# Performance work log

Hardware: AMD Instinct MI355X
Metric: run time of the kernel (lower is better)

Reference implementation:

```python
import math
import jax, jax.numpy as jnp
import numpy as np


def _bilinear_maps_sample(kv_feats, shapes_wh, start_ids, locs, map_ids):
    """Bilinear sampling from concatenated multi-level 2D maps.

    kv_feats: [BH, S, C] flattened (row-major, per level) feature maps
    shapes_wh: [L, 2] int (W, H) per level
    start_ids: [L] int start offset of each level in S
    locs: [BH, M, 2] normalized (x, y) in [0, 1]
    map_ids: [BH, M] int level index per sample
    returns [BH, M, C]
    """
    wh = shapes_wh[map_ids]                      # [BH, M, 2]
    W = wh[..., 0]
    H = wh[..., 1]
    start = start_ids[map_ids]                   # [BH, M]
    Wf = W.astype(locs.dtype)
    Hf = H.astype(locs.dtype)
    x = locs[..., 0] * Wf - 0.5                  # align_corners=False convention
    y = locs[..., 1] * Hf - 0.5
    x0 = jnp.floor(x)
    y0 = jnp.floor(y)
    out = jnp.zeros(locs.shape[:-1] + (kv_feats.shape[-1],), kv_feats.dtype)
    for dx in (0, 1):
        for dy in (0, 1):
            xi = x0 + dx
            yi = y0 + dy
            w = (1.0 - jnp.abs(x - xi)) * (1.0 - jnp.abs(y - yi))
            valid = (xi >= 0) & (xi < Wf) & (yi >= 0) & (yi < Hf)
            xi_c = jnp.clip(xi, 0, Wf - 1).astype(jnp.int32)
            yi_c = jnp.clip(yi, 0, Hf - 1).astype(jnp.int32)
            idx = start + yi_c * W + xi_c        # [BH, M]
            f = jnp.take_along_axis(kv_feats, idx[..., None], axis=1)
            out = out + jnp.where(valid, w, 0.0)[..., None] * f
    return out


def setup_inputs() -> dict:
    key = jax.random.key(0)
    ks = jax.random.split(key, 10)
    B, N, L, Hh, P = 2, 2048, 5, 8, 4
    in_size, sample_size = 256, 256
    qk_size, value_size = 256, 256
    kv_size = qk_size + value_size

    shapes = np.array([[128, 128], [64, 64], [32, 32], [16, 16], [8, 8]], np.int32)  # (H, W)
    flat = (shapes[:, 0] * shapes[:, 1]).astype(np.int64)
    start = np.concatenate([[0], np.cumsum(flat)[:-1]]).astype(np.int32)
    S = int(flat.sum())  # 21824

    # sampling_offsets bias: canonical Deformable-DETR grid init
    thetas = np.arange(Hh, dtype=np.float32) * (2.0 * math.pi / Hh)
    grid = np.stack([np.cos(thetas), np.sin(thetas)], axis=1)
    grid = grid / np.abs(grid).max(axis=1, keepdims=True)
    grid = np.tile(grid.reshape(Hh, 1, 1, 2), (1, L, 1, 1))
    sizes = np.arange(1, P + 1, dtype=np.float32).reshape(1, 1, P, 1)
    b_off = (sizes * grid).reshape(-1)           # [H*L*P*2]

    def lin(k, out_d, in_d):
        return jax.random.normal(k, (out_d, in_d), jnp.float32) * (1.0 / math.sqrt(in_d))

    return {
        "in_feats": jax.random.normal(ks[0], (B, N, in_size), jnp.float32),
        "sample_priors": jax.random.uniform(ks[1], (B, N, L, 2), jnp.float32),
        "sample_feats": jax.random.normal(ks[2], (B, S, sample_size), jnp.float32),
        "sample_map_shapes": jnp.asarray(shapes),
        "sample_map_start_ids": jnp.asarray(start),
        "W_off": jax.random.normal(ks[3], (Hh * L * P * 2, in_size), jnp.float32) * 0.02,
        "b_off": jnp.asarray(b_off),
        "W_q": lin(ks[4], qk_size, in_size),
        "b_q": jnp.zeros((qk_size,), jnp.float32),
        "W_kv": lin(ks[5], kv_size, sample_size),
        "b_kv": jnp.zeros((kv_size,), jnp.float32),
        "point_encs": jax.random.normal(ks[6], (Hh, L * P, qk_size // Hh), jnp.float32) * 0.02,
        "W_out": lin(ks[7], in_size, value_size),
        "b_out": jnp.zeros((in_size,), jnp.float32),
    }


def reference(in_feats, sample_priors, sample_feats, sample_map_shapes,
              sample_map_start_ids, W_off, b_off, W_q, b_q, W_kv, b_kv,
              point_encs, W_out, b_out):
    B, N = in_feats.shape[:2]
    Hh, LP, dqk = point_encs.shape
    L = sample_map_shapes.shape[0]
    P = LP // L

    # sampling offsets + locations (priors last dim == 2 path)
    off = (in_feats @ W_off.T + b_off).reshape(B, N, Hh, L, P, 2)
    shapes_wh = sample_map_shapes[:, ::-1]                      # fliplr -> (W, H)
    norm = shapes_wh.astype(in_feats.dtype)[None, None, None, :, None, :]
    locs = sample_priors[:, :, None, :, None, :] + off / norm    # [B,N,H,L,P,2]

    q = (in_feats @ W_q.T + b_q).reshape(B, N, Hh, dqk)
    kv = sample_feats @ W_kv.T + b_kv                            # [B,S,kv_size]
    ck = kv.shape[-1] // Hh
    kv = kv.reshape(B, -1, Hh, ck).transpose(0, 2, 1, 3).reshape(B * Hh, -1, ck)

    locs = locs.transpose(0, 2, 1, 3, 4, 5).reshape(B * Hh, N * L * P, 2)
    map_ids = jnp.broadcast_to(jnp.arange(L, dtype=jnp.int32)[None, None, :, None],
                               (B * Hh, N, L, P)).reshape(B * Hh, -1)

    sampled = _bilinear_maps_sample(kv, shapes_wh, sample_map_start_ids, locs, map_ids)
    sampled = sampled.reshape(B, Hh, N, LP, ck).transpose(0, 2, 1, 3, 4)  # [B,N,H,LP,ck]

    keys = sampled[..., :dqk] + point_encs                       # [B,N,H,LP,dqk]
    vals = sampled[..., dqk:]                                    # [B,N,H,LP,cv]
    attn = jax.nn.softmax(
        jnp.einsum('bnhd,bnhpd->bnhp', q / math.sqrt(dqk), keys), axis=-1)
    weighted = jnp.einsum('bnhp,bnhpd->bnhd', attn, vals).reshape(B, N, -1)
    return weighted @ W_out.T + b_out
```

## Files before the change

### kernel.cpp

```cpp
#include <hip/hip_runtime.h>
#include <cstddef>

#define B_  2
#define N_  2048
#define L_  5
#define HH  8
#define P_  4
#define S_  21824
#define DQK 32

using bf16x8 = __attribute__((ext_vector_type(8))) short;
using f32x4  = __attribute__((ext_vector_type(4))) float;
using us8    = __attribute__((ext_vector_type(8))) unsigned short;
using h2     = __attribute__((ext_vector_type(2))) _Float16;

__device__ __forceinline__ unsigned short f2b(float f) {
  unsigned u = __builtin_bit_cast(unsigned, f);
  u += 0x7FFFu + ((u >> 16) & 1u);
  return (unsigned short)(u >> 16);
}
__device__ __forceinline__ float b2f(unsigned short h) {
  return __builtin_bit_cast(float, ((unsigned)h) << 16);
}
__device__ __forceinline__ unsigned cvtpk(float lo, float hi) {
  unsigned r;
  asm("v_cvt_pk_bf16_f32 %0, %1, %2" : "=v"(r) : "v"(lo), "v"(hi));
  return r;
}
__device__ __forceinline__ h2 pkrtz(float a, float b) {
  return __builtin_bit_cast(h2, __builtin_amdgcn_cvt_pkrtz(a, b));
}
__device__ __forceinline__ unsigned pkrtz_u(float a, float b) {
  return __builtin_bit_cast(unsigned, __builtin_amdgcn_cvt_pkrtz(a, b));
}
__device__ __forceinline__ h2 u2h(unsigned u) { return __builtin_bit_cast(h2, u); }

__device__ __forceinline__ void gld_lds16(const void* g, void* l) {
  __builtin_amdgcn_global_load_lds(
      (const __attribute__((address_space(1))) unsigned int*)g,
      (__attribute__((address_space(3))) unsigned int*)l, 16, 0, 0);
}

template <int CTRL>
__device__ __forceinline__ float dppadd(float v) {
  const int x = __builtin_bit_cast(int, v);
  return v + __builtin_bit_cast(float,
      __builtin_amdgcn_update_dpp(x, x, CTRL, 0xF, 0xF, false));
}

#define E0 1396736
#define E1 1527808
#define E2 1658880
#define E3 1675264
#define E4 1683456
#define E5 1691648
#define E6 1703936
#define E7 1716224

__device__ __forceinline__ void cvt8_plain(const float* s, unsigned short* d, int u) {
  const float4 a = ((const float4*)s)[2 * u];
  const float4 b = ((const float4*)s)[2 * u + 1];
  us8 o;
  o[0] = f2b(a.x); o[1] = f2b(a.y); o[2] = f2b(a.z); o[3] = f2b(a.w);
  o[4] = f2b(b.x); o[5] = f2b(b.y); o[6] = f2b(b.z); o[7] = f2b(b.w);
  ((us8*)d)[u] = o;
}
__device__ __forceinline__ unsigned short f2b_lo(float x) {
  return f2b(x - b2f(f2b(x)));
}
__device__ __forceinline__ void cvt8_lo(const float* s, unsigned short* d, int u) {
  const float4 a = ((const float4*)s)[2 * u];
  const float4 b = ((const float4*)s)[2 * u + 1];
  us8 o;
  o[0] = f2b_lo(a.x); o[1] = f2b_lo(a.y); o[2] = f2b_lo(a.z); o[3] = f2b_lo(a.w);
  o[4] = f2b_lo(b.x); o[5] = f2b_lo(b.y); o[6] = f2b_lo(b.z); o[7] = f2b_lo(b.w);
  ((us8*)d)[u] = o;
}

__global__ __launch_bounds__(256) void cvt_all(
    const float* __restrict__ sfeats, const float* __restrict__ in_feats,
    const float* __restrict__ W_kv, const float* __restrict__ W_q,
    const float* __restrict__ W_out, const float* __restrict__ W_off,
    unsigned short* __restrict__ sf_bf, unsigned short* __restrict__ if_hi,
    unsigned short* __restrict__ if_lo, unsigned short* __restrict__ wkv_bf,
    unsigned short* __restrict__ wq_bf, unsigned short* __restrict__ wout_bf,
    unsigned short* __restrict__ woff_hi, unsigned short* __restrict__ woff_lo) {
  const int i = blockIdx.x * 256 + threadIdx.x;
  if      (i < E0) cvt8_plain(sfeats, sf_bf, i);
  else if (i < E1) cvt8_plain(in_feats, if_hi, i - E0);
  else if (i < E2) cvt8_lo(in_feats, if_lo, i - E1);
  else if (i < E3) cvt8_plain(W_kv, wkv_bf, i - E2);
  else if (i < E4) cvt8_plain(W_q, wq_bf, i - E3);
  else if (i < E5) cvt8_plain(W_out, wout_bf, i - E4);
  else if (i < E6) {
    const int u = i - E5;
    if ((u >> 5) < 320) cvt8_plain(W_off, woff_hi, u);
    else ((us8*)woff_hi)[u] = (us8)0;
  } else {
    const int u = i - E6;
    if ((u >> 5) < 320) cvt8_lo(W_off, woff_lo, u);
    else ((us8*)woff_lo)[u] = (us8)0;
  }
}

__device__ __forceinline__ void mfma_compute(
    const unsigned short* As, const unsigned short* Bs,
    int wr, int wc, int fr, int fq, f32x4 (&acc)[4][4]) {
#pragma unroll
  for (int kk = 0; kk < 2; ++kk) {
    bf16x8 af[4], bfv[4];
#pragma unroll
    for (int i = 0; i < 4; ++i) {
      const int ar = wr * 64 + i * 16 + fr;
      const int cha = (kk * 4 + fq) ^ (ar & 7);
      af[i] = *(const bf16x8*)(As + ar * 64 + cha * 8);
      const int br = wc * 64 + i * 16 + fr;
      const int chb = (kk * 4 + fq) ^ (br & 7);
      bfv[i] = *(const bf16x8*)(Bs + br * 64 + chb * 8);
    }
#pragma unroll
    for (int i = 0; i < 4; ++i)
#pragma unroll
      for (int j = 0; j < 4; ++j)
        acc[i][j] = __builtin_amdgcn_mfma_f32_16x16x32_bf16(
            af[i], bfv[j], acc[i][j], 0, 0, 0);
  }
}

__device__ __forceinline__ void mfma_tile_bf16(
    const unsigned short* __restrict__ Ap, const unsigned short* __restrict__ Wp,
    unsigned short* As, unsigned short* Bs,
    int row0, int col0, int wv, int wr, int wc, int fr, int fq,
    int srow, int sch, f32x4 (&acc)[4][4]) {
  for (int k0 = 0; k0 < 256; k0 += 64) {
#pragma unroll
    for (int i = 0; i < 4; ++i) {
      const int r = i * 32 + srow;
      const int ca = sch ^ (r & 7);
      gld_lds16(Ap + (size_t)(row0 + r) * 256 + k0 + ca * 8,
                As + (size_t)(i * 32 + wv * 8) * 64);
      gld_lds16(Wp + (size_t)(col0 + r) * 256 + k0 + ca * 8,
                Bs + (size_t)(i * 32 + wv * 8) * 64);
    }
    __syncthreads();
    mfma_compute(As, Bs, wr, wc, fr, fq, acc);
    __syncthreads();
  }
}

__global__ __launch_bounds__(256) void ubergemm(
    const unsigned short* __restrict__ sf_bf,
    const unsigned short* __restrict__ wkv_bf,
    const unsigned short* __restrict__ if_hi,
    const unsigned short* __restrict__ if_lo,
    const unsigned short* __restrict__ woff_hi,
    const unsigned short* __restrict__ woff_lo,
    const unsigned short* __restrict__ wq_bf,
    const float* __restrict__ b_kv, const float* __restrict__ b_off,
    const float* __restrict__ b_q,
    unsigned short* __restrict__ kvt, float* __restrict__ offb,
    float* __restrict__ qb) {
  __shared__ __align__(16) unsigned short lds[128 * 128];

  const int tid = threadIdx.x;
  const int lane = tid & 63;
  const int wv = tid >> 6;
  const int wr = wv >> 1, wc = wv & 1;
  const int fr = lane & 15, fq = lane >> 4;
  const int bx = blockIdx.x;

  f32x4 acc[4][4] = {};

  if (bx >= 160) {
    const int t = bx - 160;
    const int x = t & 7;
    const int idx = t >> 3;
    const int c = idx & 3;
    const int g = (idx >> 2) * 8 + x;
    if (g >= 341) return;
    const int row0 = g * 128;
    const int col0 = c * 128;

    unsigned short* Ab[2] = {lds, lds + 4096};
    unsigned short* Bb[2] = {lds + 8192, lds + 12288};

#define KV_STAGE(KK, BUF)                                                     \
    {                                                                         \
      _Pragma("unroll")                                                       \
      for (int ld = 0; ld < 2; ++ld) {                                        \
        const int ci = ld * 256 + tid;                                        \
        const int rw = ci >> 2, cc = ci & 3;                                  \
        const int ca = cc ^ (rw & 3);                                         \
        gld_lds16(sf_bf + (size_t)(row0 + rw) * 256 + (KK) * 32 + ca * 8,     \
                  Ab[BUF] + (size_t)(ld * 256 + wv * 64) * 8);                \
        gld_lds16(wkv_bf + (size_t)(col0 + rw) * 256 + (KK) * 32 + ca * 8,    \
                  Bb[BUF] + (size_t)(ld * 256 + wv * 64) * 8);                \
      }                                                                       \
    }

    KV_STAGE(0, 0);
#pragma unroll
    for (int k = 0; k < 8; ++k) {
      if (k < 7) {
        KV_STAGE(k + 1, (k + 1) & 1);
        asm volatile("s_waitcnt vmcnt(4)" ::: "memory");
      } else {
        asm volatile("s_waitcnt vmcnt(0)" ::: "memory");
      }
      __builtin_amdgcn_s_barrier();
      __builtin_amdgcn_sched_barrier(0);
      const unsigned short* Ac = Ab[k & 1];
      const unsigned short* Bc = Bb[k & 1];
      bf16x8 af[4], bfv[4];
#pragma unroll
      for (int i = 0; i < 4; ++i) {
        const int ar = wr * 64 + i * 16 + fr;
        af[i] = *(const bf16x8*)(Ac + (ar * 4 + (fq ^ (ar & 3))) * 8);
      }
#pragma unroll
      for (int j = 0; j < 4; ++j) {
        const int nr = wc * 64 + j * 16 + fr;
        bfv[j] = *(const bf16x8*)(Bc + (nr * 4 + (fq ^ (nr & 3))) * 8);
      }
#pragma unroll
      for (int j = 0; j < 4; ++j)
#pragma unroll
        for (int i = 0; i < 4; ++i)
          acc[j][i] = __builtin_amdgcn_mfma_f32_16x16x32_bf16(
              bfv[j], af[i], acc[j][i], 0, 0, 0);
      __builtin_amdgcn_s_barrier();
    }
#undef KV_STAGE

#pragma unroll
    for (int j = 0; j < 4; ++j) {
      const int c0 = col0 + wc * 64 + j * 16 + fq * 4;
      const float4 bb = *(const float4*)(b_kv + c0);
      const int h = c0 >> 6;
      const int cc = c0 & 63;
#pragma unroll
      for (int i = 0; i < 4; ++i) {
        const int sl = row0 + wr * 64 + i * 16 + fr;
        const int b = (sl >= S_) ? 1 : 0;
        const int s = sl - b * S_;
        unsigned* dst = (unsigned*)(kvt + ((size_t)(b * HH + h) * S_ + s) * 64 + cc);
        dst[0] = pkrtz_u(acc[j][i][0] + bb.x, acc[j][i][1] + bb.y);
        dst[1] = pkrtz_u(acc[j][i][2] + bb.z, acc[j][i][3] + bb.w);
      }
    }
    return;
  }

  unsigned short* As = lds;
  unsigned short* Bs = lds + 128 * 64;
  const int srow = tid >> 3;
  const int sch = tid & 7;
  int row0, col0, ldc, nbias;
  const float* bias;
  float* Cf;
  if (bx < 96) {
    col0 = (bx % 3) * 128; row0 = (bx / 3) * 128;
    bias = b_off; Cf = offb; ldc = 384; nbias = 320;
    mfma_tile_bf16(if_hi, woff_hi, As, Bs, row0, col0, wv, wr, wc, fr, fq, srow, sch, acc);
    mfma_tile_bf16(if_hi, woff_lo, As, Bs, row0, col0, wv, wr, wc, fr, fq, srow, sch, acc);
    mfma_tile_bf16(if_lo, woff_hi, As, Bs, row0, col0, wv, wr, wc, fr, fq, srow, sch, acc);
  } else {
    const int t = bx - 96;
    col0 = (t & 1) * 128; row0 = (t >> 1) * 128;
    bias = b_q; Cf = qb; ldc = 256; nbias = 256;
    mfma_tile_bf16(if_hi, wq_bf, As, Bs, row0, col0, wv, wr, wc, fr, fq, srow, sch, acc);
  }

#pragma unroll
  for (int j = 0; j < 4; ++j) {
    const int n = col0 + wc * 64 + j * 16 + fr;
    const float bv = (n < nbias) ? bias[n] : 0.f;
#pragma unroll
    for (int i = 0; i < 4; ++i) {
      const int mbase = row0 + wr * 64 + i * 16 + fq * 4;
#pragma unroll
      for (int r = 0; r < 4; ++r)
        Cf[(size_t)(mbase + r) * ldc + n] = acc[i][j][r] + bv;
    }
  }
}

__global__ __launch_bounds__(256) void gemm_out(
    const unsigned short* __restrict__ A, const unsigned short* __restrict__ Wt,
    const float* __restrict__ bias, float* __restrict__ C) {
  __shared__ __align__(16) unsigned short As[128 * 64];
  __shared__ __align__(16) unsigned short Bs[128 * 64];
  const int tid = threadIdx.x;
  const int lane = tid & 63;
  const int wv = tid >> 6;
  const int wr = wv >> 1, wc = wv & 1;
  const int fr = lane & 15, fq = lane >> 4;
  const int row0 = blockIdx.y * 128, col0 = blockIdx.x * 128;
  const int srow = tid >> 3, sch = tid & 7;
  f32x4 acc[4][4] = {};
  mfma_tile_bf16(A, Wt, As, Bs, row0, col0, wv, wr, wc, fr, fq, srow, sch, acc);
#pragma unroll
  for (int j = 0; j < 4; ++j) {
    const int n = col0 + wc * 64 + j * 16 + fr;
    const float bv = bias[n];
#pragma unroll
    for (int i = 0; i < 4; ++i) {
      const int mbase = row0 + wr * 64 + i * 16 + fq * 4;
#pragma unroll
      for (int r = 0; r < 4; ++r)
        C[(size_t)(mbase + r) * 256 + n] = acc[i][j][r] + bv;
    }
  }
}

__global__ __launch_bounds__(256) void sample_attn6(
    const unsigned short* __restrict__ kvt,
    const float* __restrict__ offb,
    const float* __restrict__ qb,
    const float* __restrict__ priors,
    const int* __restrict__ shapes,
    const int* __restrict__ starts,
    const float* __restrict__ pencs,
    unsigned short* __restrict__ wtd) {
  __shared__ __align__(16) int pbuf[4][20][8];
  const int wv = threadIdx.x >> 6;
  const int lane = threadIdx.x & 63;
  const int beta = blockIdx.x;
  const int sig = (beta & 7) * 2 + (beta >> 12);
  const int chunk = (beta >> 3) & 511;
  const int h = sig & 7;
  const int b = sig >> 3;
  const int bn = b * N_ + chunk * 4 + wv;
  const int j = lane & 31;
  const int half = lane >> 5;

  if (lane < 20) {
    const int pp = lane;
    const int l = pp >> 2;
    const float2 oxy = *(const float2*)(offb + (size_t)bn * 384 + h * 40 + pp * 2);
    const float2 pxy = *(const float2*)(priors + ((size_t)bn * 5 + l) * 2);
    const int Wd = shapes[l * 2 + 1];
    const int Hd = shapes[l * 2 + 0];
    const int st = starts[l];
    const float Wf = (float)Wd, Hf = (float)Hd;
    const float x = (pxy.x + oxy.x / Wf) * Wf - 0.5f;
    const float y = (pxy.y + oxy.y / Hf) * Hf - 0.5f;
    const float x0f = floorf(x), y0f = floorf(y);
    const float fx = x - x0f, fy = y - y0f;
    const int xi = (int)x0f, yi = (int)y0f;
    int a[4]; unsigned wpk[4];
#pragma unroll
    for (int dy = 0; dy < 2; ++dy)
#pragma unroll
      for (int dx = 0; dx < 2; ++dx) {
        const int xc = xi + dx, yc = yi + dy;
        const bool valid = (xc >= 0) & (xc < Wd) & (yc >= 0) & (yc < Hd);
        const float wt = (dx ? fx : 1.f - fx) * (dy ? fy : 1.f - fy);
        const float wm = valid ? wt : 0.f;
        const int xcc = min(max(xc, 0), Wd - 1);
        const int ycc = min(max(yc, 0), Hd - 1);
        a[dy * 2 + dx] = (st + ycc * Wd + xcc) * 32;
        wpk[dy * 2 + dx] = pkrtz_u(wm, wm);
      }
    *(int4*)&pbuf[wv][pp][0] = make_int4(a[0], a[1], a[2], a[3]);
    *(int4*)&pbuf[wv][pp][4] =
        make_int4((int)wpk[0], (int)wpk[1], (int)wpk[2], (int)wpk[3]);
  }

  const int jc = j & 15;
  float2 q2 = *(const float2*)(qb + (size_t)bn * 256 + h * DQK + 2 * jc);
  q2.x *= 0.17677669529663687f;
  q2.y *= 0.17677669529663687f;
  const h2 qpk = pkrtz(q2.x, q2.y);
  float qpe[10];
#pragma unroll
  for (int i = 0; i < 10; ++i) {
    const float2 pe = *(const float2*)(
        pencs + ((size_t)h * 20 + 2 * i + half) * DQK + 2 * jc);
    qpe[i] = q2.x * pe.x + q2.y * pe.y;
  }

  const unsigned* kvd = (const unsigned*)(kvt + (size_t)(b * HH + h) * (S_ * 64));

  uint4 wwp[5];
  unsigned g[5][4];
#pragma unroll
  for (int i = 0; i < 5; ++i) {
    const int4 aa = *(const int4*)&pbuf[wv][2 * i + half][0];
    wwp[i] = *(const uint4*)&pbuf[wv][2 * i + half][4];
    g[i][0] = kvd[(unsigned)aa.x + j];
    g[i][1] = kvd[(unsigned)aa.y + j];
    g[i][2] = kvd[(unsigned)aa.z + j];
    g[i][3] = kvd[(unsigned)aa.w + j];
  }

  h2 sam[10];
  float lg[10];
#pragma unroll
  for (int i = 0; i < 10; ++i) {
    const int s = i % 5;
    const uint4 wt = wwp[s];
    const unsigned g0 = g[s][0], g1 = g[s][1], g2 = g[s][2], g3 = g[s][3];
    if (i < 5) {
      const int4 aa = *(const int4*)&pbuf[wv][2 * (i + 5) + half][0];
      wwp[s] = *(const uint4*)&pbuf[wv][2 * (i + 5) + half][4];
      g[s][0] = kvd[(unsigned)aa.x + j];
      g[s][1] = kvd[(unsigned)aa.y + j];
      g[s][2] = kvd[(unsigned)aa.z + j];
      g[s][3] = kvd[(unsigned)aa.w + j];
    }
    h2 v = u2h(wt.x) * u2h(g0);
    v = u2h(wt.y) * u2h(g1) + v;
    v = u2h(wt.z) * u2h(g2) + v;
    v = u2h(wt.w) * u2h(g3) + v;
    sam[i] = v;
    float part = (j < 16) ? __builtin_amdgcn_fdot2(qpk, v, qpe[i], false) : 0.f;
    part = dppadd<0xB1>(part);
    part = dppadd<0x4E>(part);
    part = dppadd<0x124>(part);
    part = dppadd<0x128>(part);
    lg[i] = part + __shfl_xor(part, 16, 64);
  }

  float mx = lg[0];
#pragma unroll
  for (int i = 1; i < 10; ++i) mx = fmaxf(mx, lg[i]);
  mx = fmaxf(mx, __shfl_xor(mx, 32, 64));
  float se = 0.f;
#pragma unroll
  for (int i = 0; i < 10; ++i) {
    lg[i] = __expf(lg[i] - mx);
    se += lg[i];
  }
  se += __shfl_xor(se, 32, 64);
  const float inv = 1.f / se;

  float ax = 0.f, ay = 0.f;
#pragma unroll
  for (int i = 0; i < 10; ++i) {
    ax = fmaf(lg[i], (float)sam[i][0], ax);
    ay = fmaf(lg[i], (float)sam[i][1], ay);
  }
  ax += __shfl_xor(ax, 32, 64);
  ay += __shfl_xor(ay, 32, 64);

  if (half == 0 && j >= 16) {
    const unsigned u = (unsigned)f2b(ax * inv) | ((unsigned)f2b(ay * inv) << 16);
    ((unsigned*)wtd)[(size_t)bn * 128 + h * 16 + (j - 16)] = u;
  }
}

extern "C" void kernel_launch(void* const* d_in, const int* in_sizes, int n_in,
                              void* d_out, int out_size, void* d_ws, size_t ws_size,
                              hipStream_t stream) {
  const float* in_feats = (const float*)d_in[0];
  const float* priors   = (const float*)d_in[1];
  const float* sfeats   = (const float*)d_in[2];
  const int*   shapes   = (const int*)d_in[3];
  const int*   starts   = (const int*)d_in[4];
  const float* W_off    = (const float*)d_in[5];
  const float* b_off    = (const float*)d_in[6];
  const float* W_q      = (const float*)d_in[7];
  const float* b_q      = (const float*)d_in[8];
  const float* W_kv     = (const float*)d_in[9];
  const float* b_kv     = (const float*)d_in[10];
  const float* pencs    = (const float*)d_in[11];
  const float* W_out    = (const float*)d_in[12];
  const float* b_out    = (const float*)d_in[13];
  float* out = (float*)d_out;

  char* w = (char*)d_ws;
  unsigned short* kvt = (unsigned short*)w;
  w += (size_t)B_ * HH * S_ * 64 * 2;
  unsigned short* sf_bf = (unsigned short*)w;
  w += (size_t)B_ * S_ * 256 * 2;
  unsigned short* if_hi = (unsigned short*)w; w += (size_t)4096 * 256 * 2;
  unsigned short* if_lo = (unsigned short*)w; w += (size_t)4096 * 256 * 2;
  unsigned short* wkv_bf = (unsigned short*)w;  w += (size_t)512 * 256 * 2;
  unsigned short* wq_bf  = (unsigned short*)w;  w += (size_t)256 * 256 * 2;
  unsigned short* wout_bf = (unsigned short*)w; w += (size_t)256 * 256 * 2;
  unsigned short* woff_hi = (unsigned short*)w; w += (size_t)384 * 256 * 2;
  unsigned short* woff_lo = (unsigned short*)w; w += (size_t)384 * 256 * 2;
  float* offb = (float*)w;  w += (size_t)4096 * 384 * 4;
  float* qb   = (float*)w;  w += (size_t)4096 * 256 * 4;
  unsigned short* wtd_bf = (unsigned short*)w; w += (size_t)4096 * 256 * 2;

  cvt_all<<<E7 / 256, 256, 0, stream>>>(
      sfeats, in_feats, W_kv, W_q, W_out, W_off,
      sf_bf, if_hi, if_lo, wkv_bf, wq_bf, wout_bf, woff_hi, woff_lo);

  ubergemm<<<1536, 256, 0, stream>>>(
      sf_bf, wkv_bf, if_hi, if_lo, woff_hi, woff_lo, wq_bf,
      b_kv, b_off, b_q, kvt, offb, qb);

  sample_attn6<<<(B_ * N_ * HH) / 4, 256, 0, stream>>>(
      kvt, offb, qb, priors, shapes, starts, pencs, wtd_bf);

  gemm_out<<<dim3(2, 32), 256, 0, stream>>>(wtd_bf, wout_bf, b_out, out);
}
```

Measured before the change: 83.45 us.

## Fuse sample_feats bf16 conversion into KV GEMM loads from fp32

The KV projection GEMM now streams fp32 sample features straight into LDS and converts them to bf16 while building MFMA fragments, so the separate conversion pass and its bf16 intermediate buffer are gone. The conversion kernel also produces the hi and lo parts of in_feats in one pass, and the prep grid shrinks to just weights and in_feats. The cost is doubled A-tile global traffic and LDS footprint (48KB) inside the GEMM, extra conversion ALU work in the inner loop, and possibly lower occupancy.

```diff
diff --git a/kernel.cpp b/kernel.cpp
--- a/kernel.cpp
+++ b/kernel.cpp
@@ -48,14 +48,12 @@
       __builtin_amdgcn_update_dpp(x, x, CTRL, 0xF, 0xF, false));
 }
 
-#define E0 1396736
-#define E1 1527808
-#define E2 1658880
-#define E3 1675264
-#define E4 1683456
-#define E5 1691648
-#define E6 1703936
-#define E7 1716224
+#define F0 131072
+#define F1 147456
+#define F2 155648
+#define F3 163840
+#define F4 176128
+#define F5 188416
 
 __device__ __forceinline__ void cvt8_plain(const float* s, unsigned short* d, int u) {
   const float4 a = ((const float4*)s)[2 * u];
@@ -76,28 +74,41 @@
   o[4] = f2b_lo(b.x); o[5] = f2b_lo(b.y); o[6] = f2b_lo(b.z); o[7] = f2b_lo(b.w);
   ((us8*)d)[u] = o;
 }
+__device__ __forceinline__ void cvt8_both(const float* s, unsigned short* dh,
+                                          unsigned short* dl, int u) {
+  const float4 a = ((const float4*)s)[2 * u];
+  const float4 b = ((const float4*)s)[2 * u + 1];
+  us8 oh, ol;
+  const float v[8] = {a.x, a.y, a.z, a.w, b.x, b.y, b.z, b.w};
+#pragma unroll
+  for (int k = 0; k < 8; ++k) {
+    const unsigned short hh = f2b(v[k]);
+    oh[k] = hh;
+    ol[k] = f2b(v[k] - b2f(hh));
+  }
+  ((us8*)dh)[u] = oh;
+  ((us8*)dl)[u] = ol;
+}
 
 __global__ __launch_bounds__(256) void cvt_all(
-    const float* __restrict__ sfeats, const float* __restrict__ in_feats,
-    const float* __restrict__ W_kv, const float* __restrict__ W_q,
-    const float* __restrict__ W_out, const float* __restrict__ W_off,
-    unsigned short* __restrict__ sf_bf, unsigned short* __restrict__ if_hi,
-    unsigned short* __restrict__ if_lo, unsigned short* __restrict__ wkv_bf,
-    unsigned short* __restrict__ wq_bf, unsigned short* __restrict__ wout_bf,
-    unsigned short* __restrict__ woff_hi, unsigned short* __restrict__ woff_lo) {
+    const float* __restrict__ in_feats, const float* __restrict__ W_kv,
+    const float* __restrict__ W_q, const float* __restrict__ W_out,
+    const float* __restrict__ W_off,
+    unsigned short* __restrict__ if_hi, unsigned short* __restrict__ if_lo,
+    unsigned short* __restrict__ wkv_bf, unsigned short* __restrict__ wq_bf,
+    unsigned short* __restrict__ wout_bf, unsigned short* __restrict__ woff_hi,
+    unsigned short* __restrict__ woff_lo) {
   const int i = blockIdx.x * 256 + threadIdx.x;
-  if      (i < E0) cvt8_plain(sfeats, sf_bf, i);
-  else if (i < E1) cvt8_plain(in_feats, if_hi, i - E0);
-  else if (i < E2) cvt8_lo(in_feats, if_lo, i - E1);
-  else if (i < E3) cvt8_plain(W_kv, wkv_bf, i - E2);
-  else if (i < E4) cvt8_plain(W_q, wq_bf, i - E3);
-  else if (i < E5) cvt8_plain(W_out, wout_bf, i - E4);
-  else if (i < E6) {
-    const int u = i - E5;
+  if      (i < F0) cvt8_both(in_feats, if_hi, if_lo, i);
+  else if (i < F1) cvt8_plain(W_kv, wkv_bf, i - F0);
+  else if (i < F2) cvt8_plain(W_q, wq_bf, i - F1);
+  else if (i < F3) cvt8_plain(W_out, wout_bf, i - F2);
+  else if (i < F4) {
+    const int u = i - F3;
     if ((u >> 5) < 320) cvt8_plain(W_off, woff_hi, u);
     else ((us8*)woff_hi)[u] = (us8)0;
   } else {
-    const int u = i - E6;
+    const int u = i - F4;
     if ((u >> 5) < 320) cvt8_lo(W_off, woff_lo, u);
     else ((us8*)woff_lo)[u] = (us8)0;
   }
@@ -149,7 +160,7 @@
 }
 
 __global__ __launch_bounds__(256) void ubergemm(
-    const unsigned short* __restrict__ sf_bf,
+    const float* __restrict__ sfeats,
     const unsigned short* __restrict__ wkv_bf,
     const unsigned short* __restrict__ if_hi,
     const unsigned short* __restrict__ if_lo,
@@ -160,7 +171,7 @@
     const float* __restrict__ b_q,
     unsigned short* __restrict__ kvt, float* __restrict__ offb,
     float* __restrict__ qb) {
-  __shared__ __align__(16) unsigned short lds[128 * 128];
+  __shared__ __align__(16) unsigned char ldsraw[49152];
 
   const int tid = threadIdx.x;
   const int lane = tid & 63;
@@ -181,20 +192,27 @@
     const int row0 = g * 128;
     const int col0 = c * 128;
 
-    unsigned short* Ab[2] = {lds, lds + 4096};
-    unsigned short* Bb[2] = {lds + 8192, lds + 12288};
+    float* Afb[2] = {(float*)ldsraw, (float*)(ldsraw + 16384)};
+    unsigned short* Bb[2] = {(unsigned short*)(ldsraw + 32768),
+                             (unsigned short*)(ldsraw + 40960)};
 
 #define KV_STAGE(KK, BUF)                                                     \
     {                                                                         \
       _Pragma("unroll")                                                       \
-      for (int ld = 0; ld < 2; ++ld) {                                        \
+      for (int ld = 0; ld < 4; ++ld) {             \
+        const int ci = ld * 256 + tid;                                        \
+        const int rw = ci >> 3, cc = ci & 7;                                  \
+        const int ca = cc ^ (rw & 7);                                         \
+        gld_lds16(sfeats + (size_t)(row0 + rw) * 256 + (KK) * 32 + ca * 4,    \
+                  (char*)Afb[BUF] + (ld * 4096 + wv * 1024));                 \
+      }                                                                       \
+      _Pragma("unroll")                                                       \
+      for (int ld = 0; ld < 2; ++ld) {              \
         const int ci = ld * 256 + tid;                                        \
         const int rw = ci >> 2, cc = ci & 3;                                  \
         const int ca = cc ^ (rw & 3);                                         \
-        gld_lds16(sf_bf + (size_t)(row0 + rw) * 256 + (KK) * 32 + ca * 8,     \
-                  Ab[BUF] + (size_t)(ld * 256 + wv * 64) * 8);                \
         gld_lds16(wkv_bf + (size_t)(col0 + rw) * 256 + (KK) * 32 + ca * 8,    \
-                  Bb[BUF] + (size_t)(ld * 256 + wv * 64) * 8);                \
+                  (char*)Bb[BUF] + (ld * 4096 + wv * 1024));                  \
       }                                                                       \
     }
 
@@ -203,19 +221,27 @@
     for (int k = 0; k < 8; ++k) {
       if (k < 7) {
         KV_STAGE(k + 1, (k + 1) & 1);
-        asm volatile("s_waitcnt vmcnt(4)" ::: "memory");
+        asm volatile("s_waitcnt vmcnt(6)" ::: "memory");
       } else {
         asm volatile("s_waitcnt vmcnt(0)" ::: "memory");
       }
       __builtin_amdgcn_s_barrier();
       __builtin_amdgcn_sched_barrier(0);
-      const unsigned short* Ac = Ab[k & 1];
+      const float* Ac = Afb[k & 1];
       const unsigned short* Bc = Bb[k & 1];
       bf16x8 af[4], bfv[4];
 #pragma unroll
       for (int i = 0; i < 4; ++i) {
         const int ar = wr * 64 + i * 16 + fr;
-        af[i] = *(const bf16x8*)(Ac + (ar * 4 + (fq ^ (ar & 3))) * 8);
+        const int swz = ar & 7;
+        const float4 a0 = *(const float4*)(Ac + ar * 32 + (((fq * 2) ^ swz) * 4));
+        const float4 a1 = *(const float4*)(Ac + ar * 32 + (((fq * 2 + 1) ^ swz) * 4));
+        uint4 u;
+        u.x = cvtpk(a0.x, a0.y);
+        u.y = cvtpk(a0.z, a0.w);
+        u.z = cvtpk(a1.x, a1.y);
+        u.w = cvtpk(a1.z, a1.w);
+        af[i] = __builtin_bit_cast(bf16x8, u);
       }
 #pragma unroll
       for (int j = 0; j < 4; ++j) {
@@ -251,8 +277,8 @@
     return;
   }
 
-  unsigned short* As = lds;
-  unsigned short* Bs = lds + 128 * 64;
+  unsigned short* As = (unsigned short*)ldsraw;
+  unsigned short* Bs = (unsigned short*)(ldsraw + 16384);
   const int srow = tid >> 3;
   const int sch = tid & 7;
   int row0, col0, ldc, nbias;
@@ -472,8 +498,6 @@
   char* w = (char*)d_ws;
   unsigned short* kvt = (unsigned short*)w;
   w += (size_t)B_ * HH * S_ * 64 * 2;
-  unsigned short* sf_bf = (unsigned short*)w;
-  w += (size_t)B_ * S_ * 256 * 2;
   unsigned short* if_hi = (unsigned short*)w; w += (size_t)4096 * 256 * 2;
   unsigned short* if_lo = (unsigned short*)w; w += (size_t)4096 * 256 * 2;
   unsigned short* wkv_bf = (unsigned short*)w;  w += (size_t)512 * 256 * 2;
@@ -485,12 +509,12 @@
   float* qb   = (float*)w;  w += (size_t)4096 * 256 * 4;
   unsigned short* wtd_bf = (unsigned short*)w; w += (size_t)4096 * 256 * 2;
 
-  cvt_all<<<E7 / 256, 256, 0, stream>>>(
-      sfeats, in_feats, W_kv, W_q, W_out, W_off,
-      sf_bf, if_hi, if_lo, wkv_bf, wq_bf, wout_bf, woff_hi, woff_lo);
+  cvt_all<<<F5 / 256, 256, 0, stream>>>(
+      in_feats, W_kv, W_q, W_out, W_off,
+      if_hi, if_lo, wkv_bf, wq_bf, wout_bf, woff_hi, woff_lo);
 
   ubergemm<<<1536, 256, 0, stream>>>(
-      sf_bf, wkv_bf, if_hi, if_lo, woff_hi, woff_lo, wq_bf,
+      sfeats, wkv_bf, if_hi, if_lo, woff_hi, woff_lo, wq_bf,
       b_kv, b_off, b_q, kvt, offb, qb);
 
   sample_attn6<<<(B_ * N_ * HH) / 4, 256, 0, stream>>>(
```

Measured after the change: 82.16 us (median of 2 runs). No clear change (-1.5%).
